# Optimization experiments

Measured on AMD Instinct MI355X. Metric: run time of the kernel, lower is better.

The kernel has to match this reference:

```python
import jax, jax.numpy as jnp
import numpy as np

HIDDEN = 2048
NUM_V = 16
NUM_K = 8
HK = 128
HV = 128
KCONV = 4
KEY_DIM = NUM_K * HK      # 1024
VALUE_DIM = NUM_V * HV    # 2048
CONV_DIM = 2 * KEY_DIM + VALUE_DIM  # 4096
R = NUM_V // NUM_K        # 2
L2_EPS = 1e-6
NORM_EPS = 1e-6


def setup_inputs() -> dict:
    key = jax.random.key(0)
    ks = jax.random.split(key, 8)
    s = 0.02
    return {
        "hidden_states": jax.random.normal(ks[0], (1, 1024, HIDDEN), jnp.float32),
        "w_qkvz": jax.random.normal(ks[1], (2 * KEY_DIM + 2 * VALUE_DIM, HIDDEN), jnp.float32) * s,
        "w_ba": jax.random.normal(ks[2], (2 * NUM_V, HIDDEN), jnp.float32) * s,
        "conv_w": jax.random.normal(ks[3], (CONV_DIM, KCONV), jnp.float32) * s,
        "dt_bias": jnp.ones((NUM_V,), jnp.float32),
        "A_log": jnp.log(jax.random.uniform(ks[4], (NUM_V,), jnp.float32, 1e-3, 16.0)),
        "norm_weight": jnp.ones((HV,), jnp.float32),
        "w_out": jax.random.normal(ks[5], (HIDDEN, VALUE_DIM), jnp.float32) * s,
    }


def reference(hidden_states, w_qkvz, w_ba, conv_w, dt_bias, A_log, norm_weight, w_out):
    B, T, _ = hidden_states.shape
    # --- input projections ---
    qkvz = hidden_states @ w_qkvz.T                     # [B,T,2K+2V]
    ba = hidden_states @ w_ba.T                         # [B,T,2*Hv]
    # fix_query_key_value_ordering: group by k-head, layout [hk, hk, r*hv, r*hv]
    qkvz = qkvz.reshape(B, T, NUM_K, 2 * HK + 2 * R * HV)
    q, k, v, z = jnp.split(qkvz, [HK, 2 * HK, 2 * HK + R * HV], axis=3)
    v = v.reshape(B, T, NUM_V, HV)
    z = z.reshape(B, T, NUM_V, HV)
    ba = ba.reshape(B, T, NUM_K, 2 * R)
    b = ba[..., :R].reshape(B, T, NUM_V)
    a = ba[..., R:].reshape(B, T, NUM_V)
    # --- depthwise causal conv1d + silu over concatenated q,k,v ---
    mixed = jnp.concatenate(
        [q.reshape(B, T, KEY_DIM), k.reshape(B, T, KEY_DIM), v.reshape(B, T, VALUE_DIM)], axis=-1
    )
    xc = mixed.transpose(0, 2, 1)                       # [B,C,T]
    yc = jax.lax.conv_general_dilated(
        xc, conv_w[:, None, :], (1,), [(KCONV - 1, 0)],
        feature_group_count=CONV_DIM, dimension_numbers=("NCH", "OIH", "NCH"),
    )
    yc = jax.nn.silu(yc).transpose(0, 2, 1)             # [B,T,C]
    q, k, v = jnp.split(yc, [KEY_DIM, 2 * KEY_DIM], axis=-1)
    q = q.reshape(B, T, NUM_K, HK)
    k = k.reshape(B, T, NUM_K, HK)
    v = v.reshape(B, T, NUM_V, HV)
    # --- gates ---
    beta = jax.nn.sigmoid(b)                            # [B,T,Hv]
    g = -jnp.exp(A_log) * jax.nn.softplus(a + dt_bias)  # [B,T,Hv] (log decay, <=0)
    # GQA expansion of q,k to value heads
    q = jnp.repeat(q, R, axis=2)                        # [B,T,Hv,hk]
    k = jnp.repeat(k, R, axis=2)
    # l2 norm on q,k (use_qk_l2norm_in_kernel=True)
    q = q * jax.lax.rsqrt(jnp.sum(q * q, -1, keepdims=True) + L2_EPS)
    k = k * jax.lax.rsqrt(jnp.sum(k * k, -1, keepdims=True) + L2_EPS)
    scale = HK ** -0.5
    # --- gated delta rule recurrence ---
    def step(S, xs):
        qt, kt, vt, gt, bt = xs                          # per-timestep slices
        S = S * jnp.exp(gt)[..., None, None]             # decay state [B,Hv,hk,hv]
        kv = jnp.einsum("bhk,bhkv->bhv", kt, S)          # readout at k_t
        delta = (vt - kv) * bt[..., None]                # beta-gated delta
        S = S + jnp.einsum("bhk,bhv->bhkv", kt, delta)
        o = jnp.einsum("bhk,bhkv->bhv", qt * scale, S)
        return S, o

    S0 = jnp.zeros((B, NUM_V, HK, HV), hidden_states.dtype)
    xs = (
        q.transpose(1, 0, 2, 3), k.transpose(1, 0, 2, 3), v.transpose(1, 0, 2, 3),
        g.transpose(1, 0, 2), beta.transpose(1, 0, 2),
    )
    _, o = jax.lax.scan(step, S0, xs)                   # o: [T,B,Hv,hv]
    o = o.transpose(1, 0, 2, 3)                         # [B,T,Hv,hv]
    # --- gated RMSNorm (gate applied before normalization, Mamba2/Qwen3Next style) ---
    xf = o.astype(jnp.float32) * jax.nn.silu(z.astype(jnp.float32))
    var = jnp.mean(xf * xf, -1, keepdims=True)
    xn = xf * jax.lax.rsqrt(var + NORM_EPS) * norm_weight
    # --- output projection ---
    return xn.reshape(B, T, VALUE_DIM) @ w_out.T
```

## Files before the change

kernel.cpp:

```cpp
#include <hip/hip_runtime.h>
#include <math.h>

#define T_LEN   1024
#define HIDDEN  2048
#define QKVZ_N  6144
#define VAL_DIM 2048

typedef _Float16 half8 __attribute__((ext_vector_type(8)));
typedef _Float16 half4 __attribute__((ext_vector_type(4)));
typedef _Float16 half2t __attribute__((ext_vector_type(2)));
typedef float floatx4 __attribute__((ext_vector_type(4)));

__device__ __forceinline__ float sigmoidf_(float x) { return 1.f / (1.f + expf(-x)); }

__device__ __forceinline__ void gl_lds16(const _Float16* g, _Float16* l) {
    __builtin_amdgcn_global_load_lds(
        (const __attribute__((address_space(1))) void*)g,
        (__attribute__((address_space(3))) void*)l, 16, 0, 0);
}

__global__ __launch_bounds__(256) void cvt3(const float* __restrict__ s0, _Float16* __restrict__ d0, int n0,
                                            const float* __restrict__ s1, _Float16* __restrict__ d1, int n1,
                                            const float* __restrict__ s2, _Float16* __restrict__ d2, int n2) {
    int i = blockIdx.x * 256 + threadIdx.x;
    const float* s;
    _Float16* d;
    if (i < n0) { s = s0; d = d0; }
    else if (i < n0 + n1) { s = s1; d = d1; i -= n0; }
    else if (i < n0 + n1 + n2) { s = s2; d = d2; i -= n0 + n1; }
    else return;
    const float4 v = ((const float4*)s)[i];
    half4 h;
    h[0] = (_Float16)v.x; h[1] = (_Float16)v.y;
    h[2] = (_Float16)v.z; h[3] = (_Float16)v.w;
    *(half4*)&d[i * 4] = h;
}

template <typename OutT>
__global__ __launch_bounds__(256, 2) void gemm_h16(const _Float16* __restrict__ A,
                                                   const _Float16* __restrict__ W,
                                                   OutT* __restrict__ C,
                                                   int MB, int NB, int K) {
    const int N = NB * 128;
    const int l = blockIdx.x;
    const int x = l & 7;
    const int tt = l >> 3;
    const int mb = tt % MB;
    const int nb = x + 8 * (tt / MB);
    const int m0 = mb * 64, n0 = nb * 128;

    const int t = threadIdx.x;
    const int wave = t >> 6;
    const int lane = t & 63;
    const int wr = (wave >> 1) * 32;
    const int wc = (wave & 1) * 64;
    const int l15 = lane & 15;
    const int quad = lane >> 4;

    __shared__ __align__(16) _Float16 Ah[2048];
    __shared__ __align__(16) _Float16 Bh[4096];

    const int sr = lane >> 2;
    const int skq = lane & 3;

    floatx4 acc[2][4];
#pragma unroll
    for (int i = 0; i < 2; ++i)
#pragma unroll
        for (int j = 0; j < 4; ++j) acc[i][j] = 0;

    for (int k0 = 0; k0 < K; k0 += 32) {
        __syncthreads();
        {
            const int r = wave * 16 + sr;
            const int kc = skq ^ ((r ^ (r >> 2)) & 3);
            gl_lds16(A + (size_t)(m0 + r) * K + k0 + kc * 8, &Ah[wave * 512]);
        }
#pragma unroll
        for (int p = 0; p < 2; ++p) {
            const int r = p * 64 + wave * 16 + sr;
            const int kc = skq ^ ((r ^ (r >> 2)) & 3);
            gl_lds16(W + (size_t)(n0 + r) * K + k0 + kc * 8, &Bh[p * 2048 + wave * 512]);
        }
        __syncthreads();
        half8 af[2], bf[4];
#pragma unroll
        for (int mt = 0; mt < 2; ++mt) {
            const int m = wr + mt * 16 + l15;
            af[mt] = *(const half8*)&Ah[(m * 4 + (quad ^ ((m ^ (m >> 2)) & 3))) * 8];
        }
#pragma unroll
        for (int nt = 0; nt < 4; ++nt) {
            const int n = wc + nt * 16 + l15;
            bf[nt] = *(const half8*)&Bh[(n * 4 + (quad ^ ((n ^ (n >> 2)) & 3))) * 8];
        }
#pragma unroll
        for (int mt = 0; mt < 2; ++mt)
#pragma unroll
            for (int nt = 0; nt < 4; ++nt)
                acc[mt][nt] = __builtin_amdgcn_mfma_f32_16x16x32_f16(
                    af[mt], bf[nt], acc[mt][nt], 0, 0, 0);
    }
#pragma unroll
    for (int mt = 0; mt < 2; ++mt)
#pragma unroll
        for (int nt = 0; nt < 4; ++nt) {
            const int c = n0 + wc + nt * 16 + l15;
#pragma unroll
            for (int reg = 0; reg < 4; ++reg) {
                const int r = m0 + wr + mt * 16 + quad * 4 + reg;
                C[(size_t)r * N + c] = (OutT)acc[mt][nt][reg];
            }
        }
}

__global__ __launch_bounds__(256) void gemm_ba_gates(const float* __restrict__ A,
                                                     const float* __restrict__ W,
                                                     const float* __restrict__ dt_bias,
                                                     const float* __restrict__ A_log,
                                                     float* __restrict__ lgd,
                                                     float* __restrict__ bet) {
    const int m = blockIdx.x;
    const int tid = threadIdx.x;
    const int kl = tid & 31;
    const int ng = tid >> 5;
    const float* Arow = A + (size_t)m * 2048;
    __shared__ float sba[32];

    float4 a4[16];
#pragma unroll
    for (int j = 0; j < 16; ++j)
        a4[j] = *(const float4*)(Arow + j * 128 + kl * 4);

#pragma unroll
    for (int nn = 0; nn < 4; ++nn) {
        const int n = nn * 8 + ng;
        const float* Wrow = W + (size_t)n * 2048;
        float acc = 0.f;
#pragma unroll
        for (int j = 0; j < 16; ++j) {
            const float4 w4 = *(const float4*)(Wrow + j * 128 + kl * 4);
            acc = fmaf(a4[j].x, w4.x, acc);
            acc = fmaf(a4[j].y, w4.y, acc);
            acc = fmaf(a4[j].z, w4.z, acc);
            acc = fmaf(a4[j].w, w4.w, acc);
        }
        acc += __shfl_xor(acc, 1, 64);
        acc += __shfl_xor(acc, 2, 64);
        acc += __shfl_xor(acc, 4, 64);
        acc += __shfl_xor(acc, 8, 64);
        acc += __shfl_xor(acc, 16, 64);
        if (kl == 0) sba[n] = acc;
    }
    __syncthreads();
    if (tid < 16) {
        const int vh = tid, kh = vh >> 1, r = vh & 1;
        const float b = sba[kh * 4 + r];
        const float a = sba[kh * 4 + 2 + r];
        bet[m * 16 + vh] = 1.f / (1.f + expf(-b));
        const float xx = a + dt_bias[vh];
        const float sp = (xx > 0.f) ? (xx + log1pf(expf(-xx))) : log1pf(expf(xx));
        lgd[m * 16 + vh] = -expf(A_log[vh]) * sp;
    }
}

__global__ __launch_bounds__(512) void conv_silu_l2(const _Float16* __restrict__ qkvz,
                                                    const float* __restrict__ conv_w,
                                                    _Float16* __restrict__ qc,
                                                    _Float16* __restrict__ kc,
                                                    _Float16* __restrict__ vc) {
    const int t = blockIdx.x;
    const int c = threadIdx.x * 8;
    int col;
    _Float16* dst;
    bool isqk;
    float extra = 1.f;
    if (c < 1024) {
        col = ((c >> 7) * 768) + (c & 127);
        dst = qc + t * 1024 + c;
        isqk = true;
        extra = 0.08838834764831845f;
    } else if (c < 2048) {
        const int cc = c - 1024;
        col = ((cc >> 7) * 768) + 128 + (cc & 127);
        dst = kc + t * 1024 + cc;
        isqk = true;
    } else {
        const int cc = c - 2048;
        col = ((cc >> 8) * 768) + 256 + (cc & 255);
        dst = vc + (size_t)t * 2048 + cc;
        isqk = false;
    }
    const size_t gb = (size_t)t * QKVZ_N + col;
    const half8 x3 = *(const half8*)(qkvz + gb);
    half8 x2, x1, x0;
    if (t >= 1) x2 = *(const half8*)(qkvz + gb - QKVZ_N);
    if (t >= 2) x1 = *(const half8*)(qkvz + gb - 2 * (size_t)QKVZ_N);
    if (t >= 3) x0 = *(const half8*)(qkvz + gb - 3 * (size_t)QKVZ_N);

    float y[8];
    float ss = 0.f;
#pragma unroll
    for (int u = 0; u < 8; ++u) {
        const float4 wv = *(const float4*)(conv_w + (c + u) * 4);
        float acc = (float)x3[u] * wv.w;
        if (t >= 1) acc = fmaf((float)x2[u], wv.z, acc);
        if (t >= 2) acc = fmaf((float)x1[u], wv.y, acc);
        if (t >= 3) acc = fmaf((float)x0[u], wv.x, acc);
        acc = acc * (1.f / (1.f + expf(-acc)));
        y[u] = acc;
        ss = fmaf(acc, acc, ss);
    }
    half8 ov;
    if (isqk) {
        ss += __shfl_xor(ss, 1, 64);
        ss += __shfl_xor(ss, 2, 64);
        ss += __shfl_xor(ss, 4, 64);
        ss += __shfl_xor(ss, 8, 64);
        const float r = rsqrtf(ss + 1e-6f) * extra;
#pragma unroll
        for (int u = 0; u < 8; ++u) ov[u] = (_Float16)(y[u] * r);
    } else {
#pragma unroll
        for (int u = 0; u < 8; ++u) ov[u] = (_Float16)y[u];
    }
    *(half8*)dst = ov;
}

__global__ __launch_bounds__(256) void chunk_prep(
    const _Float16* __restrict__ qch, const _Float16* __restrict__ kch,
    const _Float16* __restrict__ vch, const float* __restrict__ lgd,
    const float* __restrict__ bet, _Float16* __restrict__ CH,
    float* __restrict__ gamC) {
    const int blk = blockIdx.x;
    const int c = blk >> 4, h = blk & 15, kh = h >> 1;
    const int c0 = c * 64;
    const int tid = threadIdx.x, lane = tid & 63, wave = tid >> 6;
    const int l15 = lane & 15, quad = lane >> 4;

    __shared__ __align__(16) _Float16 Ksh[8192];
    __shared__ __align__(16) _Float16 Qsh[8192];
    __shared__ float Amat[64 * 65];
    __shared__ float Gs[64], Bets[64], Gam[64];

    {
        const int t = tid >> 2, kc0 = (tid & 3) * 4;
        const size_t gb = (size_t)(c0 + t) * 1024 + kh * 128;
#pragma unroll
        for (int i = 0; i < 4; ++i) {
            const int kc = kc0 + i;
            half8 kv = *(const half8*)(kch + gb + kc * 8);
            half8 qv = *(const half8*)(qch + gb + kc * 8);
            const int chl = t * 16 + (kc ^ (t & 15));
            *(half8*)&Ksh[chl * 8] = kv;
            *(half8*)&Qsh[chl * 8] = qv;
        }
    }
    if (tid < 64) {
        float g = lgd[(size_t)(c0 + tid) * 16 + h];
#pragma unroll
        for (int off = 1; off < 64; off <<= 1) {
            float y = __shfl_up(g, off, 64);
            if (tid >= off) g += y;
        }
        Gs[tid] = g;
        Gam[tid] = expf(g);
        Bets[tid] = bet[(size_t)(c0 + tid) * 16 + h];
    }
    __syncthreads();

    _Float16* CHb = CH + (size_t)(c * 16 + h) * 36864;
    _Float16* Ug = CHb;
    _Float16* Wtg = CHb + 8192;
    _Float16* Khg = CHb + 16384;
    _Float16* Qgg = CHb + 24576;
    _Float16* Lg = CHb + 32768;

    {
        floatx4 accKK[4], accQK[4];
#pragma unroll
        for (int tt = 0; tt < 4; ++tt) { accKK[tt] = 0; accQK[tt] = 0; }
        half8 bfK[4];
#pragma unroll
        for (int ks = 0; ks < 4; ++ks) {
            const int i = wave * 16 + l15;
            const int kc = ks * 4 + quad;
            bfK[ks] = *(const half8*)&Ksh[(i * 16 + (kc ^ (i & 15))) * 8];
        }
#pragma unroll
        for (int tt = 0; tt < 4; ++tt) {
            const int t = tt * 16 + l15;
#pragma unroll
            for (int ks = 0; ks < 4; ++ks) {
                const int kc = ks * 4 + quad;
                const int chl = (t * 16 + (kc ^ (t & 15))) * 8;
                half8 afK = *(const half8*)&Ksh[chl];
                half8 afQ = *(const half8*)&Qsh[chl];
                accKK[tt] = __builtin_amdgcn_mfma_f32_16x16x32_f16(afK, bfK[ks], accKK[tt], 0, 0, 0);
                accQK[tt] = __builtin_amdgcn_mfma_f32_16x16x32_f16(afQ, bfK[ks], accQK[tt], 0, 0, 0);
            }
        }
        const int ii = wave * 16 + l15;
        const float Gi = Gs[ii];
#pragma unroll
        for (int tt = 0; tt < 4; ++tt)
#pragma unroll
            for (int r = 0; r < 4; ++r) {
                const int t = tt * 16 + quad * 4 + r;
                const float Gt = Gs[t];
                const float ratio = (ii <= t) ? expf(Gt - Gi) : 0.f;
                if (ii < t) Amat[t * 65 + ii] = Bets[t] * ratio * accKK[tt][r];
                Lg[t * 64 + ii] = (_Float16)((ii <= t) ? ratio * accQK[tt][r] : 0.f);
            }
    }
    __syncthreads();

    {
        const int j = tid;
        float x[64];
        if (j < 128) {
#pragma unroll
            for (int t = 0; t < 64; ++t)
                x[t] = Bets[t] * (float)vch[(size_t)(c0 + t) * 2048 + h * 128 + j];
        } else {
            const int k = j - 128;
#pragma unroll
            for (int t = 0; t < 64; ++t) {
                const int chl = t * 16 + ((k >> 3) ^ (t & 15));
                x[t] = Bets[t] * Gam[t] * (float)Ksh[chl * 8 + (k & 7)];
            }
        }
#pragma unroll
        for (int t = 1; t < 64; ++t) {
            float acc = 0.f;
#pragma unroll
            for (int i = 0; i < t; ++i) acc = fmaf(Amat[t * 65 + i], x[i], acc);
            x[t] -= acc;
        }
        if (j < 128) {
#pragma unroll
            for (int t = 0; t < 64; t += 4) {
                half4 w4;
                w4[0] = (_Float16)x[t]; w4[1] = (_Float16)x[t + 1];
                w4[2] = (_Float16)x[t + 2]; w4[3] = (_Float16)x[t + 3];
                *(half4*)&Wtg[j * 64 + t] = w4;
            }
        } else {
            const int k = j - 128;
#pragma unroll
            for (int t = 0; t < 64; ++t) Ug[t * 128 + k] = (_Float16)x[t];
        }
    }

    {
        const float g63 = Gs[63];
        const int k = tid >> 1, cb = (tid & 1) * 32;
#pragma unroll
        for (int cc = 0; cc < 32; cc += 4) {
            half4 o4;
#pragma unroll
            for (int u = 0; u < 4; ++u) {
                const int ci = cb + cc + u;
                const int chl = ci * 16 + ((k >> 3) ^ (ci & 15));
                o4[u] = (_Float16)(expf(g63 - Gs[ci]) * (float)Ksh[chl * 8 + (k & 7)]);
            }
            *(half4*)&Khg[k * 64 + cb + cc] = o4;
        }
        const int cq = tid >> 2, kb = (tid & 3) * 4;
        const float gam = Gam[cq];
#pragma unroll
        for (int kc = 0; kc < 4; ++kc) {
            const int kcc = kb + kc;
            half8 q8 = *(const half8*)&Qsh[(cq * 16 + (kcc ^ (cq & 15))) * 8];
            half8 s8;
#pragma unroll
            for (int u = 0; u < 8; ++u) s8[u] = (_Float16)(gam * (float)q8[u]);
            *(half8*)&Qgg[cq * 128 + kcc * 8] = s8;
        }
        if (tid == 0) gamC[c * 16 + h] = Gam[63];
    }
}

__global__ __launch_bounds__(256) void chunk_scan(const _Float16* __restrict__ CH,
                                                  const float* __restrict__ gamC,
                                                  float* __restrict__ o) {
    const int h = blockIdx.x >> 1, vs = blockIdx.x & 1;
    const int tid = threadIdx.x, lane = tid & 63, wave = tid >> 6;
    const int l15 = lane & 15, quad = lane >> 4;
    const int vrow = wave * 16 + l15;

    __shared__ __align__(16) _Float16 Sh[8192];
    __shared__ __align__(16) _Float16 Dt[4096];
    __shared__ __align__(16) _Float16 LUg[8704];
    __shared__ __align__(16) _Float16 LWt[4608];
    __shared__ __align__(16) _Float16 LKh[9216];
    __shared__ __align__(16) _Float16 LQg[8704];
    __shared__ __align__(16) _Float16 LLg[4608];

    floatx4 Sacc[8];
#pragma unroll
    for (int kt = 0; kt < 8; ++kt) Sacc[kt] = 0;
    for (int i = tid; i < 1024; i += 256) *(int4*)&Sh[i * 8] = make_int4(0, 0, 0, 0);
    __syncthreads();

    for (int c = 0; c < 16; ++c) {
        const _Float16* CHb = CH + (size_t)(c * 16 + h) * 36864;
        {
            const int4* src = (const int4*)CHb;
#pragma unroll
            for (int i = 0; i < 4; ++i) {
                const int idx = tid + i * 256;
                *(int4*)&LUg[((idx >> 4) * 17 + (idx & 15)) * 8] = src[idx];
            }
        }
        {
            const int4* src = (const int4*)(CHb + 8192 + vs * 4096);
#pragma unroll
            for (int i = 0; i < 2; ++i) {
                const int idx = tid + i * 256;
                *(int4*)&LWt[((idx >> 3) * 9 + (idx & 7)) * 8] = src[idx];
            }
        }
        {
            const int4* src = (const int4*)(CHb + 16384);
#pragma unroll
            for (int i = 0; i < 4; ++i) {
                const int idx = tid + i * 256;
                *(int4*)&LKh[((idx >> 3) * 9 + (idx & 7)) * 8] = src[idx];
            }
        }
        {
            const int4* src = (const int4*)(CHb + 24576);
#pragma unroll
            for (int i = 0; i < 4; ++i) {
                const int idx = tid + i * 256;
                *(int4*)&LQg[((idx >> 4) * 17 + (idx & 15)) * 8] = src[idx];
            }
        }
        {
            const int4* src = (const int4*)(CHb + 32768);
#pragma unroll
            for (int i = 0; i < 2; ++i) {
                const int idx = tid + i * 256;
                *(int4*)&LLg[((idx >> 3) * 9 + (idx & 7)) * 8] = src[idx];
            }
        }
        __syncthreads();

        half8 bs[4];
#pragma unroll
        for (int ks = 0; ks < 4; ++ks) {
            const int kc = ks * 4 + quad;
            bs[ks] = *(const half8*)&Sh[(vrow * 16 + (kc ^ (vrow & 15))) * 8];
        }
#pragma unroll
        for (int ct = 0; ct < 4; ++ct) {
            floatx4 xa = {0.f, 0.f, 0.f, 0.f};
#pragma unroll
            for (int ks = 0; ks < 4; ++ks) {
                half8 af = *(const half8*)&LUg[((ct * 16 + l15) * 17 + ks * 4 + quad) * 8];
                xa = __builtin_amdgcn_mfma_f32_16x16x32_f16(af, bs[ks], xa, 0, 0, 0);
            }
            half4 w4 = *(const half4*)&LWt[(vrow * 9 + ct * 2 + (quad >> 1)) * 8 + (quad & 1) * 4];
            half4 d4;
#pragma unroll
            for (int r = 0; r < 4; ++r) d4[r] = (_Float16)((float)w4[r] - xa[r]);
            const int cc = ct * 2 + (quad >> 1);
            *(half4*)&Dt[(vrow * 8 + (cc ^ (vrow & 7))) * 8 + (quad & 1) * 4] = d4;
        }
        half8 bd[2];
#pragma unroll
        for (int cs = 0; cs < 2; ++cs) {
            const int cc = cs * 4 + quad;
            bd[cs] = *(const half8*)&Dt[(vrow * 8 + (cc ^ (vrow & 7))) * 8];
        }
#pragma unroll
        for (int ct = 0; ct < 4; ++ct) {
            floatx4 oa = {0.f, 0.f, 0.f, 0.f};
#pragma unroll
            for (int ks = 0; ks < 4; ++ks) {
                half8 af = *(const half8*)&LQg[((ct * 16 + l15) * 17 + ks * 4 + quad) * 8];
                oa = __builtin_amdgcn_mfma_f32_16x16x32_f16(af, bs[ks], oa, 0, 0, 0);
            }
#pragma unroll
            for (int cs = 0; cs < 2; ++cs) {
                half8 af = *(const half8*)&LLg[((ct * 16 + l15) * 9 + cs * 4 + quad) * 8];
                oa = __builtin_amdgcn_mfma_f32_16x16x32_f16(af, bd[cs], oa, 0, 0, 0);
            }
            const int tg = c * 64 + ct * 16 + quad * 4;
            const int col = h * 128 + vs * 64 + vrow;
#pragma unroll
            for (int r = 0; r < 4; ++r) o[(size_t)(tg + r) * 2048 + col] = oa[r];
        }
        const float gC = gamC[c * 16 + h];
#pragma unroll
        for (int kt = 0; kt < 8; ++kt) {
#pragma unroll
            for (int r = 0; r < 4; ++r) Sacc[kt][r] *= gC;
#pragma unroll
            for (int cs = 0; cs < 2; ++cs) {
                half8 af = *(const half8*)&LKh[((kt * 16 + l15) * 9 + cs * 4 + quad) * 8];
                Sacc[kt] = __builtin_amdgcn_mfma_f32_16x16x32_f16(af, bd[cs], Sacc[kt], 0, 0, 0);
            }
        }
#pragma unroll
        for (int kt = 0; kt < 8; ++kt) {
            const int kc = kt * 2 + (quad >> 1);
            half4 s4;
#pragma unroll
            for (int r = 0; r < 4; ++r) s4[r] = (_Float16)Sacc[kt][r];
            *(half4*)&Sh[(vrow * 16 + (kc ^ (vrow & 15))) * 8 + (quad & 1) * 4] = s4;
        }
        __syncthreads();
    }
}

__global__ __launch_bounds__(64) void gated_norm(const float* __restrict__ o,
                                                 const _Float16* __restrict__ qkvz,
                                                 const float* __restrict__ nw,
                                                 _Float16* __restrict__ xn) {
    const int b = blockIdx.x;
    const int t = b >> 4;
    const int vh = b & 15;
    const int kh = vh >> 1;
    const int r = vh & 1;
    const float* op = o + (size_t)t * 2048 + vh * 128;
    const _Float16* zp = qkvz + (size_t)t * QKVZ_N + kh * 768 + 512 + r * 128;
    const int j = threadIdx.x * 2;
    const float2 ov = *(const float2*)(op + j);
    const half2t zv = *(const half2t*)(zp + j);
    const float z0 = (float)zv[0], z1 = (float)zv[1];
    const float f0 = ov.x * z0 / (1.f + expf(-z0));
    const float f1 = ov.y * z1 / (1.f + expf(-z1));
    float ss = f0 * f0 + f1 * f1;
#pragma unroll
    for (int m = 1; m < 64; m <<= 1) ss += __shfl_xor(ss, m, 64);
    const float rs = rsqrtf(ss * (1.f / 128.f) + 1e-6f);
    _Float16* xp = xn + (size_t)t * 2048 + vh * 128;
    half2t y;
    y[0] = (_Float16)(f0 * rs * nw[j]);
    y[1] = (_Float16)(f1 * rs * nw[j + 1]);
    *(half2t*)(xp + j) = y;
}

extern "C" void kernel_launch(void* const* d_in, const int* in_sizes, int n_in,
                              void* d_out, int out_size, void* d_ws, size_t ws_size,
                              hipStream_t stream) {
    const float* hidden  = (const float*)d_in[0];
    const float* w_qkvz  = (const float*)d_in[1];
    const float* w_ba    = (const float*)d_in[2];
    const float* conv_w  = (const float*)d_in[3];
    const float* dt_bias = (const float*)d_in[4];
    const float* A_log   = (const float*)d_in[5];
    const float* norm_w  = (const float*)d_in[6];
    const float* w_out   = (const float*)d_in[7];
    float* out = (float*)d_out;

    char* w = (char*)d_ws;
    _Float16*  qkvz_h = (_Float16*)(w);
    _Float16*  qch    = (_Float16*)(w + 12713984);
    _Float16*  kch    = (_Float16*)(w + 14811136);
    _Float16*  vch    = (_Float16*)(w + 16908288);
    float*     lgd    = (float*)(w + 21102592);
    float*     bet    = (float*)(w + 21168128);
    float*     gamC   = (float*)(w + 21233664);
    float*     o      = (float*)(w + 21237760);
    _Float16*  hid_h  = (_Float16*)(w + 21237760);
    _Float16*  wqk_h  = (_Float16*)(w + 29626368);
    _Float16*  CH     = (_Float16*)(w + 29626368);
    _Float16*  xn_h   = (_Float16*)(w + 29626368 + 18874368);
    _Float16*  wout_h = (_Float16*)(w + 54792192);

    const int n0 = HIDDEN * T_LEN / 4;
    const int n1 = QKVZ_N * HIDDEN / 4;
    const int n2 = VAL_DIM * HIDDEN / 4;
    cvt3<<<(n0 + n1 + n2 + 255) / 256, 256, 0, stream>>>(hidden, hid_h, n0,
                                                         w_qkvz, wqk_h, n1,
                                                         w_out, wout_h, n2);

    gemm_h16<_Float16><<<16 * 48, 256, 0, stream>>>(hid_h, wqk_h, qkvz_h, 16, 48, HIDDEN);
    gemm_ba_gates<<<T_LEN, 256, 0, stream>>>(hidden, w_ba, dt_bias, A_log, lgd, bet);
    conv_silu_l2<<<T_LEN, 512, 0, stream>>>(qkvz_h, conv_w, qch, kch, vch);
    chunk_prep<<<256, 256, 0, stream>>>(qch, kch, vch, lgd, bet, CH, gamC);
    chunk_scan<<<32, 256, 0, stream>>>(CH, gamC, o);
    gated_norm<<<T_LEN * 16, 64, 0, stream>>>(o, qkvz_h, norm_w, xn_h);
    gemm_h16<float><<<16 * 16, 256, 0, stream>>>(xn_h, wout_h, out, 16, 16, HIDDEN);
}
```

Measured before the change: 313.4 us.

## Double-buffer GEMM LDS tiles and widen K step to 64

The fp16 MFMA GEMM now stages tiles into two LDS buffers and issues the global-to-LDS loads for the next K block while computing on the current one. It also doubles the K step from 32 to 64 and changes the XOR swizzle to 8 slots per row. The aim is to hide global load latency and halve the number of barriers per K. In exchange it uses four times the LDS (48KB per block), which may lower occupancy. The code also assumes the asynchronous LDS loads have finished at the single barrier with no explicit vmcnt wait.

```diff
diff --git a/kernel.cpp b/kernel.cpp
--- a/kernel.cpp
+++ b/kernel.cpp
@@ -56,12 +56,11 @@
     const int wc = (wave & 1) * 64;
     const int l15 = lane & 15;
     const int quad = lane >> 4;
-
-    __shared__ __align__(16) _Float16 Ah[2048];
-    __shared__ __align__(16) _Float16 Bh[4096];
-
-    const int sr = lane >> 2;
-    const int skq = lane & 3;
+    const int srow = lane >> 3;
+    const int slot = lane & 7;
+
+    __shared__ __align__(16) _Float16 Ah[2][4096];
+    __shared__ __align__(16) _Float16 Bh[2][8192];
 
     floatx4 acc[2][4];
 #pragma unroll
@@ -69,37 +68,58 @@
 #pragma unroll
         for (int j = 0; j < 4; ++j) acc[i][j] = 0;
 
-    for (int k0 = 0; k0 < K; k0 += 32) {
-        __syncthreads();
-        {
-            const int r = wave * 16 + sr;
-            const int kc = skq ^ ((r ^ (r >> 2)) & 3);
-            gl_lds16(A + (size_t)(m0 + r) * K + k0 + kc * 8, &Ah[wave * 512]);
-        }
-#pragma unroll
-        for (int p = 0; p < 2; ++p) {
-            const int r = p * 64 + wave * 16 + sr;
-            const int kc = skq ^ ((r ^ (r >> 2)) & 3);
-            gl_lds16(W + (size_t)(n0 + r) * K + k0 + kc * 8, &Bh[p * 2048 + wave * 512]);
-        }
-        __syncthreads();
-        half8 af[2], bf[4];
-#pragma unroll
-        for (int mt = 0; mt < 2; ++mt) {
-            const int m = wr + mt * 16 + l15;
-            af[mt] = *(const half8*)&Ah[(m * 4 + (quad ^ ((m ^ (m >> 2)) & 3))) * 8];
-        }
-#pragma unroll
-        for (int nt = 0; nt < 4; ++nt) {
-            const int n = wc + nt * 16 + l15;
-            bf[nt] = *(const half8*)&Bh[(n * 4 + (quad ^ ((n ^ (n >> 2)) & 3))) * 8];
-        }
+    auto stage = [&](int buf, int k0) {
+#pragma unroll
+        for (int g = 0; g < 2; ++g) {
+            const int r = wave * 16 + g * 8 + srow;
+            const int kc = slot ^ (r & 7);
+            gl_lds16(A + (size_t)(m0 + r) * K + k0 + kc * 8,
+                     &Ah[buf][(wave * 128 + g * 64) * 8]);
+        }
+#pragma unroll
+        for (int g = 0; g < 4; ++g) {
+            const int r = wave * 32 + g * 8 + srow;
+            const int kc = slot ^ (r & 7);
+            gl_lds16(W + (size_t)(n0 + r) * K + k0 + kc * 8,
+                     &Bh[buf][(wave * 256 + g * 64) * 8]);
+        }
+    };
+
+    const int NIT = K >> 6;
+    stage(0, 0);
+    __syncthreads();
+    int cur = 0;
+    for (int it = 0; it < NIT; ++it) {
+        if (it + 1 < NIT) stage(cur ^ 1, (it + 1) * 64);
+        half8 af[2][2], bf[4][2];
 #pragma unroll
         for (int mt = 0; mt < 2; ++mt)
 #pragma unroll
+            for (int ks = 0; ks < 2; ++ks) {
+                const int m = wr + mt * 16 + l15;
+                const int kq = ks * 4 + quad;
+                af[mt][ks] = *(const half8*)&Ah[cur][(m * 8 + (kq ^ (m & 7))) * 8];
+            }
+#pragma unroll
+        for (int nt = 0; nt < 4; ++nt)
+#pragma unroll
+            for (int ks = 0; ks < 2; ++ks) {
+                const int n = wc + nt * 16 + l15;
+                const int kq = ks * 4 + quad;
+                bf[nt][ks] = *(const half8*)&Bh[cur][(n * 8 + (kq ^ (n & 7))) * 8];
+            }
+#pragma unroll
+        for (int mt = 0; mt < 2; ++mt)
+#pragma unroll
             for (int nt = 0; nt < 4; ++nt)
-                acc[mt][nt] = __builtin_amdgcn_mfma_f32_16x16x32_f16(
-                    af[mt], bf[nt], acc[mt][nt], 0, 0, 0);
+#pragma unroll
+                for (int ks = 0; ks < 2; ++ks)
+                    acc[mt][nt] = __builtin_amdgcn_mfma_f32_16x16x32_f16(
+                        af[mt][ks], bf[nt][ks], acc[mt][nt], 0, 0, 0);
+        if (it + 1 < NIT) {
+            __syncthreads();
+            cur ^= 1;
+        }
     }
 #pragma unroll
     for (int mt = 0; mt < 2; ++mt)
```

After: 298.9 us. -4.6%, faster.
